# Optimization experiments

Measured on AMD Instinct MI355X. Metric: run time of the kernel, lower is better.

The kernel has to match this reference:

```python
import jax, jax.numpy as jnp
import numpy as np

B, S, D = 2, 2048, 512
H, K = 8, 64  # n_heads, dim_k (== dim_v per original code)


def setup_inputs() -> dict:
    key = jax.random.key(0)
    ks = jax.random.split(key, 11)
    s = 0.02
    return {
        "query": jax.random.normal(ks[0], (B, S, D), jnp.float32),
        "key": jax.random.normal(ks[1], (B, S, D), jnp.float32),
        "value": jax.random.normal(ks[2], (B, S, D), jnp.float32),
        # per-head Dense projections (keras Dense has bias by default)
        "Wq": jax.random.normal(ks[3], (H, D, K), jnp.float32) * s,
        "bq": jnp.zeros((H, K), jnp.float32),
        "Wk": jax.random.normal(ks[4], (H, D, K), jnp.float32) * s,
        "bk": jnp.zeros((H, K), jnp.float32),
        "Wv": jax.random.normal(ks[5], (H, D, K), jnp.float32) * s,
        "bv": jnp.zeros((H, K), jnp.float32),
        "Wo": jax.random.normal(ks[6], (H * K, D), jnp.float32) * s,
        "bo": jnp.zeros((D,), jnp.float32),
    }


def reference(query, key, value, Wq, bq, Wk, bk, Wv, bv, Wo, bo):
    # per-head linear projections, vectorized over heads: [B,H,S,K]
    q = jnp.einsum("bsd,hdk->bhsk", query, Wq) + bq[:, None, :]
    k = jnp.einsum("bsd,hdk->bhsk", key, Wk) + bk[:, None, :]
    v = jnp.einsum("bsd,hdk->bhsk", value, Wv) + bv[:, None, :]
    # scaled dot-product: scores [B,H,S,S]
    scores = jnp.einsum("bhsk,bhtk->bhst", q, k) / jnp.sqrt(jnp.float32(K))
    attn = jax.nn.softmax(scores, axis=-1)
    ctx = jnp.einsum("bhst,bhtk->bhsk", attn, v)  # [B,H,S,K]
    # concat heads -> [B,S,H*K], then output projection
    ctx = jnp.transpose(ctx, (0, 2, 1, 3)).reshape(B, S, H * K)
    return ctx @ Wo + bo
```

## Files before the change

kernel.cpp:

```cpp
#include <hip/hip_runtime.h>

#define B 2
#define S 2048
#define D 512
#define H 8
#define KD 64

typedef __bf16 bf16_t;
typedef __bf16 bf16x8 __attribute__((ext_vector_type(8)));
typedef __bf16 bf16x4 __attribute__((ext_vector_type(4)));
typedef float f32x4 __attribute__((ext_vector_type(4)));

#define QSCALE 0.1803368801111204f

__device__ __forceinline__ void async_copy16(const void* g, void* l) {
    __builtin_amdgcn_global_load_lds(
        (const __attribute__((address_space(1))) void*)g,
        (__attribute__((address_space(3))) void*)l, 16, 0, 0);
}

__device__ __forceinline__ float max3f(float a, float b, float c) {
    float d;
    asm("v_max3_f32 %0, %1, %2, %3" : "=v"(d) : "v"(a), "v"(b), "v"(c));
    return d;
}

#if __has_builtin(__builtin_amdgcn_exp2f)
__device__ __forceinline__ float fexp2(float x) { return __builtin_amdgcn_exp2f(x); }
#else
__device__ __forceinline__ float fexp2(float x) {
    float r;
    asm("v_exp_f32 %0, %1\n\ts_nop 1" : "=v"(r) : "v"(x));
    return r;
}
#endif

__global__ __launch_bounds__(256) void prep_kernel(
    const float* __restrict__ Wq, const float* __restrict__ Wk,
    const float* __restrict__ Wv, const float* __restrict__ Wo,
    const float* __restrict__ qin, const float* __restrict__ kin, const float* __restrict__ vin,
    bf16_t* __restrict__ Wtq, bf16_t* __restrict__ Wtk,
    bf16_t* __restrict__ Wtv, bf16_t* __restrict__ WoT,
    bf16_t* __restrict__ xq, bf16_t* __restrict__ xk, bf16_t* __restrict__ xv)
{
    __shared__ bf16_t tl[64][72];
    const int blk = blockIdx.x, t = threadIdx.x;

    if (blk >= 256) {
        const int idx = blk - 256;
        const int mat = idx >> 10, cidx = idx & 1023;
        const float* src = (mat == 0) ? qin : (mat == 1) ? kin : vin;
        bf16_t* dst = (mat == 0) ? xq : (mat == 1) ? xk : xv;
        const size_t i8 = ((size_t)cidx * 256 + t) * 8;
        const float4 f0 = *reinterpret_cast<const float4*>(src + i8);
        const float4 f1 = *reinterpret_cast<const float4*>(src + i8 + 4);
        bf16x8 o;
        o[0] = (bf16_t)f0.x; o[1] = (bf16_t)f0.y; o[2] = (bf16_t)f0.z; o[3] = (bf16_t)f0.w;
        o[4] = (bf16_t)f1.x; o[5] = (bf16_t)f1.y; o[6] = (bf16_t)f1.z; o[7] = (bf16_t)f1.w;
        *reinterpret_cast<bf16x8*>(dst + i8) = o;
        return;
    }

    const float* src; bf16_t* dstbase;
    int ld, r0, c0;
    if (blk < 192) {
        const int mat = blk >> 6, h = (blk & 63) >> 3, dt = blk & 7;
        const float* W = (mat == 0) ? Wq : (mat == 1) ? Wk : Wv;
        bf16_t* Wt = (mat == 0) ? Wtq : (mat == 1) ? Wtk : Wtv;
        src = W + (size_t)h * D * KD; dstbase = Wt + (size_t)h * KD * D;
        ld = KD; r0 = dt * 64; c0 = 0;
    } else {
        const int kt = (blk - 192) >> 3, nt = (blk - 192) & 7;
        src = Wo; dstbase = WoT;
        ld = D; r0 = kt * 64; c0 = nt * 64;
    }

    {
        const int r = t >> 2, cq = (t & 3) * 16;
        const float* sp = src + (size_t)(r0 + r) * ld + c0 + cq;
#pragma unroll
        for (int q = 0; q < 4; ++q) {
            const float4 f = *reinterpret_cast<const float4*>(sp + q * 4);
            tl[r][cq + q * 4 + 0] = (bf16_t)f.x; tl[r][cq + q * 4 + 1] = (bf16_t)f.y;
            tl[r][cq + q * 4 + 2] = (bf16_t)f.z; tl[r][cq + q * 4 + 3] = (bf16_t)f.w;
        }
    }
    __syncthreads();
    {
        const int cc = t >> 2, rq = (t & 3) * 16;
        bf16x8 o0, o1;
#pragma unroll
        for (int j = 0; j < 8; ++j) { o0[j] = tl[rq + j][cc]; o1[j] = tl[rq + 8 + j][cc]; }
        bf16_t* dp = dstbase + (size_t)(c0 + cc) * 512 + r0 + rq;
        *reinterpret_cast<bf16x8*>(dp) = o0;
        *reinterpret_cast<bf16x8*>(dp + 8) = o1;
    }
}

__device__ __forceinline__ void gemm_tile(
    const bf16_t* __restrict__ A, const bf16_t* __restrict__ Bt,
    int row0, int n0, char* lds, f32x4 (&acc)[2][2])
{
    const int tid = threadIdx.x, wave = tid >> 6, lane = tid & 63;
    const int g = lane >> 4, c = lane & 15;

    const int srow8 = lane >> 3, sslot = lane & 7;
    const bf16_t* asrc[2]; const bf16_t* bsrc[2];
#pragma unroll
    for (int j = 0; j < 2; ++j) {
        const int r = wave * 16 + j * 8 + srow8;
        const int ys = (r & 7) ^ (((r >> 3) & 1) << 2);
        asrc[j] = A + (size_t)(row0 + r) * 512 + ((sslot ^ ys) << 3);
        bsrc[j] = Bt + (size_t)(n0 + r) * 512 + ((sslot ^ ys) << 3);
    }
    const int adst = wave * 2048;
    const int bdst = 8192 + wave * 2048;

    const int ysr = (c & 7) ^ (((c >> 3) & 1) << 2);
    const int wm = wave >> 1, wn = wave & 1;
    int ard[2], brd[2];
#pragma unroll
    for (int f = 0; f < 2; ++f) {
        ard[f] = (wm * 32 + f * 16 + c) * 128;
        brd[f] = 8192 + (wn * 32 + f * 16 + c) * 128;
    }

#define GSTAGE(bufi, kt)                                                       \
    do { char* bp = lds + (bufi) * 16384;                                      \
        _Pragma("unroll") for (int j = 0; j < 2; ++j) {                        \
            async_copy16(asrc[j] + (kt) * 64, bp + adst + j * 1024);           \
            async_copy16(bsrc[j] + (kt) * 64, bp + bdst + j * 1024);           \
        }                                                                      \
    } while (0)

    int buf = 0;
    GSTAGE(0, 0);
    __syncthreads();
#pragma unroll 1
    for (int kt = 0; kt < 8; ++kt) {
        if (kt < 7) GSTAGE(buf ^ 1, kt + 1);
        const char* bp = lds + buf * 16384;
        __builtin_amdgcn_s_setprio(1);
#pragma unroll
        for (int ksub = 0; ksub < 2; ++ksub) {
            const int so = (((ksub << 2) | g) ^ ysr) << 4;
            bf16x8 bfr[2];
#pragma unroll
            for (int nf = 0; nf < 2; ++nf)
                bfr[nf] = *reinterpret_cast<const bf16x8*>(bp + brd[nf] + so);
#pragma unroll
            for (int mf = 0; mf < 2; ++mf) {
                const bf16x8 afr = *reinterpret_cast<const bf16x8*>(bp + ard[mf] + so);
                acc[mf][0] = __builtin_amdgcn_mfma_f32_16x16x32_bf16(afr, bfr[0], acc[mf][0], 0, 0, 0);
                acc[mf][1] = __builtin_amdgcn_mfma_f32_16x16x32_bf16(afr, bfr[1], acc[mf][1], 0, 0, 0);
            }
        }
        __builtin_amdgcn_s_setprio(0);
        __syncthreads();
        buf ^= 1;
    }
#undef GSTAGE
}

__global__ __launch_bounds__(256) void qkv_kernel(
    const bf16_t* __restrict__ xq, const bf16_t* __restrict__ xk, const bf16_t* __restrict__ xv,
    const bf16_t* __restrict__ Wtq, const bf16_t* __restrict__ Wtk, const bf16_t* __restrict__ Wtv,
    const float* __restrict__ bq, const float* __restrict__ bk, const float* __restrict__ bv,
    bf16_t* __restrict__ Qo, bf16_t* __restrict__ Ko, bf16_t* __restrict__ VTo)
{
    __shared__ char lds[2][16384];

    const int mat = blockIdx.y;
    const bf16_t* A    = (mat == 0) ? xq  : (mat == 1) ? xk  : xv;
    const bf16_t* Bt   = (mat == 0) ? Wtq : (mat == 1) ? Wtk : Wtv;
    const float* bias  = (mat == 0) ? bq  : (mat == 1) ? bk  : bv;
    const float scale  = (mat == 0) ? QSCALE : 1.0f;

    const int mtile = blockIdx.x & 63;
    const int ntile = blockIdx.x >> 6;
    const int row0 = mtile * 64, n0 = ntile * 64;

    const int lane = threadIdx.x & 63;
    const int g = lane >> 4, c = lane & 15;
    const int wave = threadIdx.x >> 6, wm = wave >> 1, wn = wave & 1;

    const f32x4 zero = {0.f, 0.f, 0.f, 0.f};
    f32x4 acc[2][2] = {{zero, zero}, {zero, zero}};
    gemm_tile(A, Bt, row0, n0, &lds[0][0], acc);

#pragma unroll
    for (int mf = 0; mf < 2; ++mf)
#pragma unroll
        for (int nf = 0; nf < 2; ++nf) {
            const int n = n0 + wn * 32 + nf * 16 + c;
            const int h = n >> 6, col = n & 63;
            const float bval = bias[n];
            const int rowb = row0 + wm * 32 + mf * 16 + 4 * g;
            const int b = rowb >> 11, s0 = rowb & 2047;
            const int bh = b * H + h;
            if (mat < 2) {
                bf16_t* outp = (mat == 0) ? Qo : Ko;
#pragma unroll
                for (int i = 0; i < 4; ++i)
                    outp[((size_t)bh * S + s0 + i) * KD + col] =
                        (bf16_t)((acc[mf][nf][i] + bval) * scale);
            } else {
                bf16x4 o;
#pragma unroll
                for (int i = 0; i < 4; ++i) o[i] = (bf16_t)(acc[mf][nf][i] + bval);
                *reinterpret_cast<bf16x4*>(VTo + ((size_t)bh * KD + col) * S + s0) = o;
            }
        }
}

template <int SPLIT>
__global__ __launch_bounds__(512) void attn_kernel(
    const bf16_t* __restrict__ Q, const bf16_t* __restrict__ Km,
    const bf16_t* __restrict__ VT,
    bf16_t* __restrict__ CTX, bf16_t* __restrict__ Opart, float* __restrict__ ML)
{
    __shared__ char kv_lds[2][16384];

    const int hw = blockIdx.x;
    const int xcd = hw & 7;
    const int idx = hw >> 3;
    const int bh = xcd * 2 + (idx >= 16 * SPLIT ? 1 : 0);
    const int r2 = idx & (16 * SPLIT - 1);
    const int chunk = r2 >> 4;
    const int stile = r2 & 15;
    const int b = bh >> 3, h = bh & (H - 1);

    const int tid = threadIdx.x, wave = tid >> 6, lane = tid & 63;
    const int g = lane >> 4, c = lane & 15;
    const int q0 = stile * 128 + wave * 16;
    const int kvbeg = chunk * (S / SPLIT);
    const int NT = (S / SPLIT) / 64;

    const bf16_t* kg = Km + (size_t)bh * S * KD;
    const bf16_t* vg = VT + (size_t)bh * KD * S;

    const bf16_t* qp = Q + ((size_t)bh * S + q0 + c) * KD;
    const bf16x8 qlo = *reinterpret_cast<const bf16x8*>(qp + g * 8);
    const bf16x8 qhi = *reinterpret_cast<const bf16x8*>(qp + 32 + g * 8);

    bf16x8 ones;
#pragma unroll
    for (int i = 0; i < 8; ++i) ones[i] = (bf16_t)1.0f;

    int koff[4][2], voff[4][2];
#pragma unroll
    for (int tt = 0; tt < 4; ++tt) {
        const int row = 8 * (c >> 2) + (c & 3) + 4 * (tt & 1) + 32 * (tt >> 1);
        const int ys = (row & 7) ^ (((row >> 3) & 1) << 2);
        koff[tt][0] = row * 128 + ((g * 16) ^ (ys << 4));
        koff[tt][1] = row * 128 + ((64 + g * 16) ^ (ys << 4));
    }
#pragma unroll
    for (int ct = 0; ct < 4; ++ct) {
        const int row = ct * 16 + c;
        const int ys = (row & 7) ^ (((row >> 3) & 1) << 2);
        voff[ct][0] = 8192 + row * 128 + ((g * 16) ^ (ys << 4));
        voff[ct][1] = 8192 + row * 128 + ((64 + g * 16) ^ (ys << 4));
    }

    const int srow = lane >> 3, sslot = lane & 7;
    const int kwv = wave & 3;
    const int krow0a = kwv * 16, krow0b = kwv * 16 + 8;
    const int rowa = krow0a + srow, rowb = krow0b + srow;
    const int ysa = (rowa & 7) ^ (((rowa >> 3) & 1) << 2);
    const int ysb = (rowb & 7) ^ (((rowb >> 3) & 1) << 2);
    const int ssa = sslot ^ ysa, ssb = sslot ^ ysb;

    const f32x4 zero = {0.f, 0.f, 0.f, 0.f};
    f32x4 acc[4] = {zero, zero, zero, zero};
    f32x4 accl = zero;
    float m_run = -1e30f;

#define STAGE(bufidx, kv0)                                                        \
    do {                                                                          \
        char* bp = kv_lds[0] + (bufidx) * 16384;                                  \
        if (wave < 4) {                                                           \
            async_copy16(kg + (size_t)((kv0) + rowa) * KD + ssa * 8, bp + krow0a * 128); \
            async_copy16(kg + (size_t)((kv0) + rowb) * KD + ssb * 8, bp + krow0b * 128); \
        } else {                                                                  \
            async_copy16(vg + (size_t)rowa * S + (kv0) + ssa * 8, bp + 8192 + krow0a * 128); \
            async_copy16(vg + (size_t)rowb * S + (kv0) + ssb * 8, bp + 8192 + krow0b * 128); \
        }                                                                         \
    } while (0)

    STAGE(0, kvbeg);
    __syncthreads();

    int buf = 0;
    for (int t = 0; t < NT; ++t) {
        if (t < NT - 1) STAGE(buf ^ 1, kvbeg + (t + 1) * 64);
        const char* kb = kv_lds[0] + buf * 16384;

        f32x4 sc[4];
        __builtin_amdgcn_s_setprio(1);
#pragma unroll
        for (int tt = 0; tt < 4; ++tt) {
            const bf16x8 k0f = *reinterpret_cast<const bf16x8*>(kb + koff[tt][0]);
            const bf16x8 k1f = *reinterpret_cast<const bf16x8*>(kb + koff[tt][1]);
            f32x4 z = zero;
            z = __builtin_amdgcn_mfma_f32_16x16x32_bf16(k0f, qlo, z, 0, 0, 0);
            sc[tt] = __builtin_amdgcn_mfma_f32_16x16x32_bf16(k1f, qhi, z, 0, 0, 0);
        }
        __builtin_amdgcn_s_setprio(0);

        const float m0 = max3f(sc[0][0], sc[0][1], sc[0][2]);
        const float m1 = max3f(sc[0][3], sc[1][0], sc[1][1]);
        const float m2 = max3f(sc[1][2], sc[1][3], sc[2][0]);
        const float m3 = max3f(sc[2][1], sc[2][2], sc[2][3]);
        const float m4 = max3f(sc[3][0], sc[3][1], sc[3][2]);
        float pm = fmaxf(max3f(max3f(m0, m1, m2), m3, m4), sc[3][3]);
        if (!__all(pm <= m_run + 8.0f)) {
            pm = fmaxf(pm, __shfl_xor(pm, 16));
            pm = fmaxf(pm, __shfl_xor(pm, 32));
            const float mn = fmaxf(m_run, pm);
            const float fs = fexp2(m_run - mn);
            m_run = mn;
            accl = accl * fs;
#pragma unroll
            for (int ct = 0; ct < 4; ++ct) acc[ct] = acc[ct] * fs;
        }

        bf16x8 f0, f1;
#pragma unroll
        for (int i = 0; i < 4; ++i) {
            f0[i]     = (bf16_t)fexp2(sc[0][i] - m_run);
            f0[4 + i] = (bf16_t)fexp2(sc[1][i] - m_run);
            f1[i]     = (bf16_t)fexp2(sc[2][i] - m_run);
            f1[4 + i] = (bf16_t)fexp2(sc[3][i] - m_run);
        }

        __builtin_amdgcn_s_setprio(1);
        accl = __builtin_amdgcn_mfma_f32_16x16x32_bf16(ones, f0, accl, 0, 0, 0);
        accl = __builtin_amdgcn_mfma_f32_16x16x32_bf16(ones, f1, accl, 0, 0, 0);
#pragma unroll
        for (int ct = 0; ct < 4; ++ct) {
            const bf16x8 v0f = *reinterpret_cast<const bf16x8*>(kb + voff[ct][0]);
            const bf16x8 v1f = *reinterpret_cast<const bf16x8*>(kb + voff[ct][1]);
            acc[ct] = __builtin_amdgcn_mfma_f32_16x16x32_bf16(v0f, f0, acc[ct], 0, 0, 0);
            acc[ct] = __builtin_amdgcn_mfma_f32_16x16x32_bf16(v1f, f1, acc[ct], 0, 0, 0);
        }
        __builtin_amdgcn_s_setprio(0);

        __syncthreads();
        buf ^= 1;
    }
#undef STAGE

    const float l_tot = accl[0];

    if constexpr (SPLIT == 1) {
        const float inv = 1.0f / l_tot;
        bf16_t* crow = CTX + ((size_t)b * S + q0 + c) * 512 + h * 64;
#pragma unroll
        for (int ct = 0; ct < 4; ++ct) {
            bf16x4 o;
#pragma unroll
            for (int i = 0; i < 4; ++i) o[i] = (bf16_t)(acc[ct][i] * inv);
            *reinterpret_cast<bf16x4*>(crow + ct * 16 + 4 * g) = o;
        }
    } else {
        const size_t prow = (size_t)(chunk * 16 + bh) * 2048 + q0 + c;
        bf16_t* orow = Opart + prow * 64;
#pragma unroll
        for (int ct = 0; ct < 4; ++ct) {
            bf16x4 o;
#pragma unroll
            for (int i = 0; i < 4; ++i) o[i] = (bf16_t)acc[ct][i];
            *reinterpret_cast<bf16x4*>(orow + ct * 16 + 4 * g) = o;
        }
        if (g == 0) {
            float2 ml; ml.x = m_run; ml.y = l_tot;
            *reinterpret_cast<float2*>(ML + prow * 2) = ml;
        }
    }
}

template <int SPLIT>
__global__ __launch_bounds__(256) void combine_kernel(
    const bf16_t* __restrict__ Opart, const float* __restrict__ ML,
    bf16_t* __restrict__ CTX)
{
    const int gid = blockIdx.x * 256 + threadIdx.x;
    const int d4 = gid & 15, rowh = gid >> 4;
    const int bh = rowh >> 11, s = rowh & 2047;
    const int b = bh >> 3, h = bh & (H - 1);

    float m[SPLIT], l[SPLIT], M = -1e30f;
#pragma unroll
    for (int i = 0; i < SPLIT; ++i) {
        const float2 v = *reinterpret_cast<const float2*>(
            ML + ((size_t)(i * 16 + bh) * 2048 + s) * 2);
        m[i] = v.x; l[i] = v.y;
        M = fmaxf(M, m[i]);
    }
    f32x4 o = {0.f, 0.f, 0.f, 0.f};
    float wsum = 0.f;
#pragma unroll
    for (int i = 0; i < SPLIT; ++i) {
        const float w = fexp2(m[i] - M);
        wsum += w * l[i];
        const bf16x4 ov = *reinterpret_cast<const bf16x4*>(
            Opart + ((size_t)(i * 16 + bh) * 2048 + s) * 64 + d4 * 4);
#pragma unroll
        for (int j = 0; j < 4; ++j) o[j] += w * (float)ov[j];
    }
    const float inv = 1.0f / wsum;
    bf16x4 r;
#pragma unroll
    for (int i = 0; i < 4; ++i) r[i] = (bf16_t)(o[i] * inv);
    *reinterpret_cast<bf16x4*>(CTX + ((size_t)b * S + s) * 512 + h * 64 + d4 * 4) = r;
}

__global__ __launch_bounds__(256) void out_proj_kernel(
    const bf16_t* __restrict__ CTX,
    const bf16_t* __restrict__ WoT,
    const float* __restrict__ bo,
    float* __restrict__ out)
{
    __shared__ char lds[2][16384];

    const int mtile = blockIdx.x & 63;
    const int ntile = blockIdx.x >> 6;
    const int row0 = mtile * 64, n0 = ntile * 64;

    const int lane = threadIdx.x & 63;
    const int g = lane >> 4, c = lane & 15;
    const int wave = threadIdx.x >> 6, wm = wave >> 1, wn = wave & 1;

    const f32x4 zero = {0.f, 0.f, 0.f, 0.f};
    f32x4 acc[2][2] = {{zero, zero}, {zero, zero}};
    gemm_tile(CTX, WoT, row0, n0, &lds[0][0], acc);

#pragma unroll
    for (int mf = 0; mf < 2; ++mf)
#pragma unroll
        for (int nf = 0; nf < 2; ++nf) {
            const int n = n0 + wn * 32 + nf * 16 + c;
            const float bval = bo[n];
            const int rowb = row0 + wm * 32 + mf * 16 + 4 * g;
#pragma unroll
            for (int i = 0; i < 4; ++i)
                out[(size_t)(rowb + i) * 512 + n] = acc[mf][nf][i] + bval;
        }
}

extern "C" void kernel_launch(void* const* d_in, const int* in_sizes, int n_in,
                              void* d_out, int out_size, void* d_ws, size_t ws_size,
                              hipStream_t stream) {
    const float* query = (const float*)d_in[0];
    const float* key_  = (const float*)d_in[1];
    const float* value = (const float*)d_in[2];
    const float* Wq = (const float*)d_in[3];
    const float* bq = (const float*)d_in[4];
    const float* Wk = (const float*)d_in[5];
    const float* bk = (const float*)d_in[6];
    const float* Wv = (const float*)d_in[7];
    const float* bv = (const float*)d_in[8];
    const float* Wo = (const float*)d_in[9];
    const float* bo = (const float*)d_in[10];

    char* wsb = (char*)d_ws;
    bf16_t* Qw   = (bf16_t*)(wsb);
    bf16_t* Kw   = (bf16_t*)(wsb + (4u  << 20));
    bf16_t* VTw  = (bf16_t*)(wsb + (8u  << 20));
    bf16_t* CTXb = (bf16_t*)(wsb + (12u << 20));
    bf16_t* Wtq  = (bf16_t*)(wsb + (16u << 20));
    bf16_t* Wtk  = Wtq + 8 * 64 * 512;
    bf16_t* Wtv  = Wtk + 8 * 64 * 512;
    bf16_t* WoTw = (bf16_t*)(wsb + (18u << 20));
    bf16_t* Xq   = (bf16_t*)(wsb + (20u << 20));
    bf16_t* Xk   = (bf16_t*)(wsb + (24u << 20));
    bf16_t* Xv   = (bf16_t*)(wsb + (28u << 20));
    bf16_t* Opart = (bf16_t*)(wsb + (32u << 20));

    const int SPLIT = (ws_size >= (70ull << 20)) ? 4
                    : (ws_size >= (52ull << 20)) ? 2 : 1;

    prep_kernel<<<256 + 3072, 256, 0, stream>>>(Wq, Wk, Wv, Wo,
                                                query, key_, value,
                                                Wtq, Wtk, Wtv, WoTw,
                                                Xq, Xk, Xv);
    qkv_kernel<<<dim3(512, 3), 256, 0, stream>>>(Xq, Xk, Xv,
                                                 Wtq, Wtk, Wtv, bq, bk, bv,
                                                 Qw, Kw, VTw);

    if (SPLIT == 4) {
        float* MLp = (float*)(Opart + 4ull * 16 * 2048 * 64);
        attn_kernel<4><<<1024, 512, 0, stream>>>(Qw, Kw, VTw, CTXb, Opart, MLp);
        combine_kernel<4><<<2048, 256, 0, stream>>>(Opart, MLp, CTXb);
    } else if (SPLIT == 2) {
        float* MLp = (float*)(Opart + 2ull * 16 * 2048 * 64);
        attn_kernel<2><<<512, 512, 0, stream>>>(Qw, Kw, VTw, CTXb, Opart, MLp);
        combine_kernel<2><<<2048, 256, 0, stream>>>(Opart, MLp, CTXb);
    } else {
        attn_kernel<1><<<256, 512, 0, stream>>>(Qw, Kw, VTw, CTXb, nullptr, nullptr);
    }

    out_proj_kernel<<<512, 256, 0, stream>>>(CTXb, WoTw, bo, (float*)d_out);
}
```

Measured before the change: 65.74 us.

## Fuse split-K combine into output projection and enlarge QKV GEMM tiles

The separate combine kernel is removed. Its softmax-partial merge (max, exp-weighted sum, normalization) now runs inside the output projection while the A operand is staged into LDS, overlapped with the MFMA loop. This drops one launch and the CTX write/read round trip, at the cost of a synchronous global-load path for A and extra register pressure. The QKV projection also moves to 128x64 tiles with its own double-buffered loop, halving the grid and raising B-operand reuse per block.

After: 70.79 us. +7.7%, slower.

```diff
diff --git a/kernel.cpp b/kernel.cpp
--- a/kernel.cpp
+++ b/kernel.cpp
@@ -168,7 +168,7 @@
     const float* __restrict__ bq, const float* __restrict__ bk, const float* __restrict__ bv,
     bf16_t* __restrict__ Qo, bf16_t* __restrict__ Ko, bf16_t* __restrict__ VTo)
 {
-    __shared__ char lds[2][16384];
+    __shared__ char lds[2][24576];
 
     const int mat = blockIdx.y;
     const bf16_t* A    = (mat == 0) ? xq  : (mat == 1) ? xk  : xv;
@@ -176,26 +176,83 @@
     const float* bias  = (mat == 0) ? bq  : (mat == 1) ? bk  : bv;
     const float scale  = (mat == 0) ? QSCALE : 1.0f;
 
-    const int mtile = blockIdx.x & 63;
-    const int ntile = blockIdx.x >> 6;
-    const int row0 = mtile * 64, n0 = ntile * 64;
-
-    const int lane = threadIdx.x & 63;
+    const int mtile = blockIdx.x & 31;
+    const int ntile = blockIdx.x >> 5;
+    const int row0 = mtile * 128, n0 = ntile * 64;
+
+    const int tid = threadIdx.x, wave = tid >> 6, lane = tid & 63;
     const int g = lane >> 4, c = lane & 15;
-    const int wave = threadIdx.x >> 6, wm = wave >> 1, wn = wave & 1;
+    const int srow8 = lane >> 3, sslot = lane & 7;
+
+    const bf16_t* asrc[4]; const bf16_t* bsrc[2];
+#pragma unroll
+    for (int j = 0; j < 4; ++j) {
+        const int r = wave * 32 + j * 8 + srow8;
+        const int ys = srow8 ^ ((j & 1) << 2);
+        asrc[j] = A + (size_t)(row0 + r) * 512 + ((sslot ^ ys) << 3);
+    }
+#pragma unroll
+    for (int j = 0; j < 2; ++j) {
+        const int r = wave * 16 + j * 8 + srow8;
+        const int ys = srow8 ^ ((j & 1) << 2);
+        bsrc[j] = Bt + (size_t)(n0 + r) * 512 + ((sslot ^ ys) << 3);
+    }
+    const int adst = wave * 4096;
+    const int bdst = 16384 + wave * 2048;
+
+    const int ysr = (c & 7) ^ (((c >> 3) & 1) << 2);
+    const int wm = wave >> 1, wn = wave & 1;
+    int ard[4], brd[2];
+#pragma unroll
+    for (int f = 0; f < 4; ++f) ard[f] = (wm * 64 + f * 16 + c) * 128;
+#pragma unroll
+    for (int f = 0; f < 2; ++f) brd[f] = 16384 + (wn * 32 + f * 16 + c) * 128;
 
     const f32x4 zero = {0.f, 0.f, 0.f, 0.f};
-    f32x4 acc[2][2] = {{zero, zero}, {zero, zero}};
-    gemm_tile(A, Bt, row0, n0, &lds[0][0], acc);
-
-#pragma unroll
-    for (int mf = 0; mf < 2; ++mf)
+    f32x4 acc[4][2] = {{zero, zero}, {zero, zero}, {zero, zero}, {zero, zero}};
+
+#define QSTAGE(bufi, kt)                                                       \
+    do { char* bp = lds[bufi];                                                 \
+        _Pragma("unroll") for (int j = 0; j < 4; ++j)                          \
+            async_copy16(asrc[j] + (kt) * 64, bp + adst + j * 1024);           \
+        _Pragma("unroll") for (int j = 0; j < 2; ++j)                          \
+            async_copy16(bsrc[j] + (kt) * 64, bp + bdst + j * 1024);           \
+    } while (0)
+
+    int buf = 0;
+    QSTAGE(0, 0);
+    __syncthreads();
+#pragma unroll 1
+    for (int kt = 0; kt < 8; ++kt) {
+        if (kt < 7) QSTAGE(buf ^ 1, kt + 1);
+        const char* bp = lds[buf];
+        __builtin_amdgcn_s_setprio(1);
+#pragma unroll
+        for (int ksub = 0; ksub < 2; ++ksub) {
+            const int so = (((ksub << 2) | g) ^ ysr) << 4;
+            const bf16x8 bfr0 = *reinterpret_cast<const bf16x8*>(bp + brd[0] + so);
+            const bf16x8 bfr1 = *reinterpret_cast<const bf16x8*>(bp + brd[1] + so);
+#pragma unroll
+            for (int mf = 0; mf < 4; ++mf) {
+                const bf16x8 afr = *reinterpret_cast<const bf16x8*>(bp + ard[mf] + so);
+                acc[mf][0] = __builtin_amdgcn_mfma_f32_16x16x32_bf16(afr, bfr0, acc[mf][0], 0, 0, 0);
+                acc[mf][1] = __builtin_amdgcn_mfma_f32_16x16x32_bf16(afr, bfr1, acc[mf][1], 0, 0, 0);
+            }
+        }
+        __builtin_amdgcn_s_setprio(0);
+        __syncthreads();
+        buf ^= 1;
+    }
+#undef QSTAGE
+
+#pragma unroll
+    for (int mf = 0; mf < 4; ++mf)
 #pragma unroll
         for (int nf = 0; nf < 2; ++nf) {
             const int n = n0 + wn * 32 + nf * 16 + c;
             const int h = n >> 6, col = n & 63;
             const float bval = bias[n];
-            const int rowb = row0 + wm * 32 + mf * 16 + 4 * g;
+            const int rowb = row0 + wm * 64 + mf * 16 + 4 * g;
             const int b = rowb >> 11, s0 = rowb & 2047;
             const int bh = b * H + h;
             if (mat < 2) {
@@ -381,45 +438,10 @@
 }
 
 template <int SPLIT>
-__global__ __launch_bounds__(256) void combine_kernel(
-    const bf16_t* __restrict__ Opart, const float* __restrict__ ML,
-    bf16_t* __restrict__ CTX)
-{
-    const int gid = blockIdx.x * 256 + threadIdx.x;
-    const int d4 = gid & 15, rowh = gid >> 4;
-    const int bh = rowh >> 11, s = rowh & 2047;
-    const int b = bh >> 3, h = bh & (H - 1);
-
-    float m[SPLIT], l[SPLIT], M = -1e30f;
-#pragma unroll
-    for (int i = 0; i < SPLIT; ++i) {
-        const float2 v = *reinterpret_cast<const float2*>(
-            ML + ((size_t)(i * 16 + bh) * 2048 + s) * 2);
-        m[i] = v.x; l[i] = v.y;
-        M = fmaxf(M, m[i]);
-    }
-    f32x4 o = {0.f, 0.f, 0.f, 0.f};
-    float wsum = 0.f;
-#pragma unroll
-    for (int i = 0; i < SPLIT; ++i) {
-        const float w = fexp2(m[i] - M);
-        wsum += w * l[i];
-        const bf16x4 ov = *reinterpret_cast<const bf16x4*>(
-            Opart + ((size_t)(i * 16 + bh) * 2048 + s) * 64 + d4 * 4);
-#pragma unroll
-        for (int j = 0; j < 4; ++j) o[j] += w * (float)ov[j];
-    }
-    const float inv = 1.0f / wsum;
-    bf16x4 r;
-#pragma unroll
-    for (int i = 0; i < 4; ++i) r[i] = (bf16_t)(o[i] * inv);
-    *reinterpret_cast<bf16x4*>(CTX + ((size_t)b * S + s) * 512 + h * 64 + d4 * 4) = r;
-}
-
 __global__ __launch_bounds__(256) void out_proj_kernel(
     const bf16_t* __restrict__ CTX,
-    const bf16_t* __restrict__ WoT,
-    const float* __restrict__ bo,
+    const bf16_t* __restrict__ Opart, const float* __restrict__ ML,
+    const bf16_t* __restrict__ WoT, const float* __restrict__ bo,
     float* __restrict__ out)
 {
     __shared__ char lds[2][16384];
@@ -428,13 +450,118 @@
     const int ntile = blockIdx.x >> 6;
     const int row0 = mtile * 64, n0 = ntile * 64;
 
-    const int lane = threadIdx.x & 63;
+    const int tid = threadIdx.x, wave = tid >> 6, lane = tid & 63;
     const int g = lane >> 4, c = lane & 15;
-    const int wave = threadIdx.x >> 6, wm = wave >> 1, wn = wave & 1;
+    const int wm = wave >> 1, wn = wave & 1;
 
     const f32x4 zero = {0.f, 0.f, 0.f, 0.f};
     f32x4 acc[2][2] = {{zero, zero}, {zero, zero}};
-    gemm_tile(CTX, WoT, row0, n0, &lds[0][0], acc);
+
+    if constexpr (SPLIT == 1) {
+        gemm_tile(CTX, WoT, row0, n0, &lds[0][0], acc);
+    } else {
+        const int srow8 = lane >> 3, sslot = lane & 7;
+
+        const bf16_t* bsrc[2];
+#pragma unroll
+        for (int j = 0; j < 2; ++j) {
+            const int r = wave * 16 + j * 8 + srow8;
+            const int ys = srow8 ^ ((j & 1) << 2);
+            bsrc[j] = WoT + (size_t)(n0 + r) * 512 + ((sslot ^ ys) << 3);
+        }
+        const int bdst = 8192 + wave * 2048;
+
+        int rloc[2], ssr[2], bh8[2], ldsAoff[2];
+#pragma unroll
+        for (int j = 0; j < 2; ++j) {
+            rloc[j] = wave * 16 + j * 8 + srow8;
+            const int row = row0 + rloc[j];
+            ssr[j] = row & 2047;
+            bh8[j] = (row >> 11) * H;
+            const int ys = srow8 ^ (j << 2);
+            ldsAoff[j] = rloc[j] * 128 + ((sslot ^ ys) << 4);
+        }
+
+        const int ysr = (c & 7) ^ (((c >> 3) & 1) << 2);
+        int ard[2], brd[2];
+#pragma unroll
+        for (int f = 0; f < 2; ++f) {
+            ard[f] = (wm * 32 + f * 16 + c) * 128;
+            brd[f] = 8192 + (wn * 32 + f * 16 + c) * 128;
+        }
+
+        bf16x8 oa[2][4]; float2 mla[2][4];
+
+#define OP_LOADA(kt)                                                           \
+        do {                                                                   \
+            _Pragma("unroll") for (int j = 0; j < 2; ++j)                      \
+            _Pragma("unroll") for (int i = 0; i < SPLIT; ++i) {                \
+                const size_t prow = ((size_t)(i * 16 + bh8[j] + (kt)) * 2048 + ssr[j]); \
+                oa[j][i]  = *reinterpret_cast<const bf16x8*>(Opart + prow * 64 + sslot * 8); \
+                mla[j][i] = *reinterpret_cast<const float2*>(ML + prow * 2);   \
+            }                                                                  \
+        } while (0)
+
+#define OP_WRITEA(bufi)                                                        \
+        do {                                                                   \
+            char* bp = lds[bufi];                                              \
+            _Pragma("unroll") for (int j = 0; j < 2; ++j) {                    \
+                float M = mla[j][0].x;                                         \
+                _Pragma("unroll") for (int i = 1; i < SPLIT; ++i) M = fmaxf(M, mla[j][i].x); \
+                float w[SPLIT]; float lsum = 0.f;                              \
+                _Pragma("unroll") for (int i = 0; i < SPLIT; ++i) {            \
+                    w[i] = fexp2(mla[j][i].x - M); lsum += w[i] * mla[j][i].y; } \
+                const float inv = 1.0f / lsum;                                 \
+                bf16x8 av;                                                     \
+                _Pragma("unroll") for (int e = 0; e < 8; ++e) {                \
+                    float s = 0.f;                                             \
+                    _Pragma("unroll") for (int i = 0; i < SPLIT; ++i)          \
+                        s += w[i] * (float)oa[j][i][e];                        \
+                    av[e] = (bf16_t)(s * inv);                                 \
+                }                                                              \
+                *reinterpret_cast<bf16x8*>(bp + ldsAoff[j]) = av;              \
+            }                                                                  \
+        } while (0)
+
+#define OP_BSTAGE(bufi, kt)                                                    \
+        do { char* bp = lds[bufi];                                             \
+            _Pragma("unroll") for (int j = 0; j < 2; ++j)                      \
+                async_copy16(bsrc[j] + (kt) * 64, bp + bdst + j * 1024);       \
+        } while (0)
+
+        int buf = 0;
+        OP_BSTAGE(0, 0);
+        OP_LOADA(0);
+        OP_WRITEA(0);
+        __syncthreads();
+#pragma unroll 1
+        for (int kt = 0; kt < 8; ++kt) {
+            if (kt < 7) { OP_BSTAGE(buf ^ 1, kt + 1); OP_LOADA(kt + 1); }
+            const char* bp = lds[buf];
+            __builtin_amdgcn_s_setprio(1);
+#pragma unroll
+            for (int ksub = 0; ksub < 2; ++ksub) {
+                const int so = (((ksub << 2) | g) ^ ysr) << 4;
+                bf16x8 bfr[2];
+#pragma unroll
+                for (int nf = 0; nf < 2; ++nf)
+                    bfr[nf] = *reinterpret_cast<const bf16x8*>(bp + brd[nf] + so);
+#pragma unroll
+                for (int mf = 0; mf < 2; ++mf) {
+                    const bf16x8 afr = *reinterpret_cast<const bf16x8*>(bp + ard[mf] + so);
+                    acc[mf][0] = __builtin_amdgcn_mfma_f32_16x16x32_bf16(afr, bfr[0], acc[mf][0], 0, 0, 0);
+                    acc[mf][1] = __builtin_amdgcn_mfma_f32_16x16x32_bf16(afr, bfr[1], acc[mf][1], 0, 0, 0);
+                }
+            }
+            __builtin_amdgcn_s_setprio(0);
+            if (kt < 7) OP_WRITEA(buf ^ 1);
+            __syncthreads();
+            buf ^= 1;
+        }
+#undef OP_LOADA
+#undef OP_WRITEA
+#undef OP_BSTAGE
+    }
 
 #pragma unroll
     for (int mf = 0; mf < 2; ++mf)
@@ -485,21 +612,20 @@
                                                 query, key_, value,
                                                 Wtq, Wtk, Wtv, WoTw,
                                                 Xq, Xk, Xv);
-    qkv_kernel<<<dim3(512, 3), 256, 0, stream>>>(Xq, Xk, Xv,
+    qkv_kernel<<<dim3(256, 3), 256, 0, stream>>>(Xq, Xk, Xv,
                                                  Wtq, Wtk, Wtv, bq, bk, bv,
                                                  Qw, Kw, VTw);
 
     if (SPLIT == 4) {
         float* MLp = (float*)(Opart + 4ull * 16 * 2048 * 64);
         attn_kernel<4><<<1024, 512, 0, stream>>>(Qw, Kw, VTw, CTXb, Opart, MLp);
-        combine_kernel<4><<<2048, 256, 0, stream>>>(Opart, MLp, CTXb);
+        out_proj_kernel<4><<<512, 256, 0, stream>>>(CTXb, Opart, MLp, WoTw, bo, (float*)d_out);
     } else if (SPLIT == 2) {
         float* MLp = (float*)(Opart + 2ull * 16 * 2048 * 64);
         attn_kernel<2><<<512, 512, 0, stream>>>(Qw, Kw, VTw, CTXb, Opart, MLp);
-        combine_kernel<2><<<2048, 256, 0, stream>>>(Opart, MLp, CTXb);
+        out_proj_kernel<2><<<512, 256, 0, stream>>>(CTXb, Opart, MLp, WoTw, bo, (float*)d_out);
     } else {
         attn_kernel<1><<<256, 512, 0, stream>>>(Qw, Kw, VTw, CTXb, nullptr, nullptr);
-    }
-
-    out_proj_kernel<<<512, 256, 0, stream>>>(CTXb, WoTw, bo, (float*)d_out);
-}
+        out_proj_kernel<1><<<512, 256, 0, stream>>>(CTXb, nullptr, nullptr, WoTw, bo, (float*)d_out);
+    }
+}
```
